# Kernel tuning notes

Measured on AMD Instinct MI355X. Metric: run time of the kernel, lower is better.

Reference implementation:

```python
import jax, jax.numpy as jnp
import numpy as np

B, CH, IMG, P = 16, 3, 384, 16
D, HEADS, DH, MLP, DEPTH = 384, 6, 64, 1536, 6
INNER = HEADS * DH
PD = P * P * 5 * CH          # SPT patch dim = 3840
GRID = IMG // P              # 24
NP = GRID * GRID             # 576 patches
SEQ = NP + 1                 # +cls = 577


def layer_norm(x, g, b, eps=1e-5):
    mu = jnp.mean(x, axis=-1, keepdims=True)
    var = jnp.var(x, axis=-1, keepdims=True)
    return (x - mu) * jax.lax.rsqrt(var + eps) * g + b


def spt_shifts(x):
    # F.pad semantics: (left,right,top,bottom) with negative = crop
    s1 = jnp.pad(x, ((0, 0), (0, 0), (0, 0), (1, 0)))[:, :, :, :-1]  # (1,-1,0,0)
    s2 = jnp.pad(x, ((0, 0), (0, 0), (0, 0), (0, 1)))[:, :, :, 1:]   # (-1,1,0,0)
    s3 = jnp.pad(x, ((0, 0), (0, 0), (1, 0), (0, 0)))[:, :, :-1, :]  # (0,0,1,-1)
    s4 = jnp.pad(x, ((0, 0), (0, 0), (0, 1), (0, 0)))[:, :, 1:, :]   # (0,0,-1,1)
    return jnp.concatenate([x, s1, s2, s3, s4], axis=1)  # [b, 5c, H, W]


def patchify(x):
    # 'b c (h p1) (w p2) -> b (h w) (p1 p2 c)'
    b, c, _, _ = x.shape
    x = x.reshape(b, c, GRID, P, GRID, P)
    x = x.transpose(0, 2, 4, 3, 5, 1)  # b h w p1 p2 c
    return x.reshape(b, GRID * GRID, P * P * c)


def setup_inputs():
    key = jax.random.key(0)
    ks = jax.random.split(key, 16)
    img = jax.random.normal(ks[0], (B, CH, IMG, IMG), jnp.float32)
    spt_g = jnp.ones((PD,), jnp.float32)
    spt_b = jnp.zeros((PD,), jnp.float32)
    spt_w = jax.random.normal(ks[1], (PD, D), jnp.float32) * (1.0 / np.sqrt(PD))
    spt_bias = jnp.zeros((D,), jnp.float32)
    pos = jax.random.normal(ks[2], (1, SEQ, D), jnp.float32) * 0.02
    cls = jax.random.normal(ks[3], (1, 1, D), jnp.float32) * 0.02
    attn_g = jnp.ones((DEPTH, D), jnp.float32)
    attn_b = jnp.zeros((DEPTH, D), jnp.float32)
    temp = jnp.full((DEPTH,), np.log(DH ** -0.5), jnp.float32)
    wqkv = jax.random.normal(ks[4], (DEPTH, D, 3 * INNER), jnp.float32) * 0.02
    wout = jax.random.normal(ks[5], (DEPTH, INNER, D), jnp.float32) * 0.02
    bout = jnp.zeros((DEPTH, D), jnp.float32)
    ff_g = jnp.ones((DEPTH, D), jnp.float32)
    ff_b = jnp.zeros((DEPTH, D), jnp.float32)
    w1 = jax.random.normal(ks[6], (DEPTH, D, MLP), jnp.float32) * 0.02
    b1 = jnp.zeros((DEPTH, MLP), jnp.float32)
    w2 = jax.random.normal(ks[7], (DEPTH, MLP, D), jnp.float32) * 0.02
    b2 = jnp.zeros((DEPTH, D), jnp.float32)
    return {"img": img, "spt_g": spt_g, "spt_b": spt_b, "spt_w": spt_w,
            "spt_bias": spt_bias, "pos": pos, "cls": cls, "attn_g": attn_g,
            "attn_b": attn_b, "temp": temp, "wqkv": wqkv, "wout": wout,
            "bout": bout, "ff_g": ff_g, "ff_b": ff_b, "w1": w1, "b1": b1,
            "w2": w2, "b2": b2}


def vit_forward(img, spt_g, spt_b, spt_w, spt_bias, pos, cls, attn_g, attn_b,
                temp, wqkv, wout, bout, ff_g, ff_b, w1, b1, w2, b2):
    # SPT patch embedding
    x = patchify(spt_shifts(img))                      # [b, NP, PD]
    x = layer_norm(x, spt_g, spt_b) @ spt_w + spt_bias  # [b, NP, D]
    b = x.shape[0]
    cls_tok = jnp.broadcast_to(cls, (b, 1, D))
    x = jnp.concatenate([cls_tok, x], axis=1) + pos[:, :SEQ]

    eye = jnp.eye(SEQ, dtype=bool)
    neg = -jnp.finfo(x.dtype).max

    def block(x, p):
        ag, ab, t, wq, wo, bo, fg, fb, W1, B1, W2, B2 = p
        h = layer_norm(x, ag, ab)
        qkv = h @ wq                                   # [b, n, 3*inner]
        q, k, v = jnp.split(qkv, 3, axis=-1)
        q = q.reshape(b, SEQ, HEADS, DH).transpose(0, 2, 1, 3)
        k = k.reshape(b, SEQ, HEADS, DH).transpose(0, 2, 1, 3)
        v = v.reshape(b, SEQ, HEADS, DH).transpose(0, 2, 1, 3)
        dots = jnp.einsum('bhid,bhjd->bhij', q, k) * jnp.exp(t)
        dots = jnp.where(eye, neg, dots)               # diagonal mask (LSA)
        attn = jax.nn.softmax(dots, axis=-1)
        out = jnp.einsum('bhij,bhjd->bhid', attn, v)
        out = out.transpose(0, 2, 1, 3).reshape(b, SEQ, INNER)
        x = out @ wo + bo + x
        h = layer_norm(x, fg, fb)
        x = jax.nn.gelu(h @ W1 + B1, approximate=False) @ W2 + B2 + x
        return x, None

    params = (attn_g, attn_b, temp, wqkv, wout, bout, ff_g, ff_b, w1, b1, w2, b2)
    x, _ = jax.lax.scan(block, x, params)
    return x


def reference(img, spt_g, spt_b, spt_w, spt_bias, pos, cls, attn_g, attn_b,
              temp, wqkv, wout, bout, ff_g, ff_b, w1, b1, w2, b2):
    return vit_forward(img, spt_g, spt_b, spt_w, spt_bias, pos, cls, attn_g,
                       attn_b, temp, wqkv, wout, bout, ff_g, ff_b, w1, b1,
                       w2, b2)
```

## Files before the change

### kernel.cpp

```cpp
#include <hip/hip_runtime.h>

typedef unsigned short ushort_t;
typedef __bf16 bf16x8 __attribute__((ext_vector_type(8)));
typedef float f32x4 __attribute__((ext_vector_type(4)));

#define SEQ_ 577
#define D_ 384
#define NTOK (16 * 577)

enum { M_QKV = 0, M_OUT, M_MLP1, M_MLP2 };

__device__ inline float b2f(ushort_t u) {
    unsigned int x = ((unsigned int)u) << 16;
    float f; __builtin_memcpy(&f, &x, 4); return f;
}
__device__ inline ushort_t f2b(float f) {
    unsigned int x; __builtin_memcpy(&x, &f, 4);
    x = x + 0x7fffu + ((x >> 16) & 1u);
    return (ushort_t)(x >> 16);
}

__device__ void transpose_tile(const float* __restrict__ src,
                               ushort_t* __restrict__ dst,
                               int ldn, int ldk, int k0, int n0)
{
    __shared__ float t[64][65];
    const int tid = threadIdx.x;
    const int c = tid & 63, rr = tid >> 6;
#pragma unroll
    for (int i = 0; i < 16; i++) {
        int kl = rr + i * 4;
        t[kl][c] = src[(size_t)(k0 + kl) * ldn + n0 + c];
    }
    __syncthreads();
#pragma unroll
    for (int i = 0; i < 16; i++) {
        int nl = rr + i * 4;
        dst[(size_t)(n0 + nl) * ldk + k0 + c] = f2b(t[c][nl]);
    }
}

__global__ __launch_bounds__(256) void prep_spt_kernel(
    const float* __restrict__ w, ushort_t* __restrict__ wt)
{
    transpose_tile(w, wt, 384, 3840, blockIdx.x * 64, blockIdx.y * 64);
}

__global__ __launch_bounds__(256) void prep_all_kernel(
    const float* __restrict__ wqkv, const float* __restrict__ wout,
    const float* __restrict__ w1, const float* __restrict__ w2,
    ushort_t* __restrict__ W6)
{
    int id = blockIdx.x;
    int l = id / 432;
    int r = id - l * 432;
    ushort_t* qkv_t  = W6 + (size_t)l * 1769472;
    ushort_t* wout_t = qkv_t + 442368;
    ushort_t* w1_t   = wout_t + 147456;
    ushort_t* w2_t   = w1_t + 589824;
    const float* wq = wqkv + (size_t)l * 442368;
    const float* wo = wout + (size_t)l * 147456;
    const float* W1 = w1 + (size_t)l * 589824;
    const float* W2 = w2 + (size_t)l * 589824;
    if (r < 108) {
        int kt = r / 18, nt = r % 18;
        transpose_tile(wq, qkv_t, 1152, 384, kt * 64, nt * 64);
    } else if (r < 144) {
        r -= 108; int kt = r / 6, nt = r % 6;
        transpose_tile(wo, wout_t, 384, 384, kt * 64, nt * 64);
    } else if (r < 288) {
        r -= 144; int kt = r / 24, nt = r % 24;
        transpose_tile(W1, w1_t, 1536, 384, kt * 64, nt * 64);
    } else {
        r -= 288; int kt = r / 6, nt = r % 6;
        transpose_tile(W2, w2_t, 384, 1536, kt * 64, nt * 64);
    }
}

template <int MODE>
__global__ __launch_bounds__(256) void gemm64(
    const ushort_t* __restrict__ A, const ushort_t* __restrict__ Bt,
    ushort_t* __restrict__ Co, float* __restrict__ resid,
    const float* __restrict__ bias,
    int M, int K, int ldc)
{
    __shared__ __align__(16) ushort_t As[2][64][40];
    __shared__ __align__(16) ushort_t Bs[2][64][40];

    const int tid = threadIdx.x;
    const int rowBase = blockIdx.y * 64;
    const int colBase = blockIdx.x * 64;
    const int nk = K >> 5;
    const int lr = tid >> 2, lk = (tid & 3) * 8;
    const int wv = tid >> 6, lane = tid & 63;
    const int wm = (wv >> 1) * 32, wn = (wv & 1) * 32;
    const int m16 = lane & 15, q4 = lane >> 4, kb = q4 * 8;

    const ushort_t* pa = A + (size_t)(rowBase + lr) * K + lk;
    const ushort_t* pb = Bt + (size_t)(colBase + lr) * K + lk;

    f32x4 acc[2][2];
#pragma unroll
    for (int i = 0; i < 2; i++)
#pragma unroll
        for (int j = 0; j < 2; j++) acc[i][j] = (f32x4){0.f, 0.f, 0.f, 0.f};

    uint4 Ua, Ub, Va, Vb;
    auto gloadU = [&](int kt) {
        Ua = *(const uint4*)(pa + kt * 32);
        Ub = *(const uint4*)(pb + kt * 32);
    };
    auto gloadV = [&](int kt) {
        Va = *(const uint4*)(pa + kt * 32);
        Vb = *(const uint4*)(pb + kt * 32);
    };
    auto swriteU = [&](int buf) {
        *(uint4*)&As[buf][lr][lk] = Ua;
        *(uint4*)&Bs[buf][lr][lk] = Ub;
    };
    auto swriteV = [&](int buf) {
        *(uint4*)&As[buf][lr][lk] = Va;
        *(uint4*)&Bs[buf][lr][lk] = Vb;
    };
    auto compute = [&](int buf) {
        bf16x8 a0 = *(const bf16x8*)&As[buf][wm + m16][kb];
        bf16x8 a1 = *(const bf16x8*)&As[buf][wm + 16 + m16][kb];
        bf16x8 b0 = *(const bf16x8*)&Bs[buf][wn + m16][kb];
        bf16x8 b1 = *(const bf16x8*)&Bs[buf][wn + 16 + m16][kb];
        acc[0][0] = __builtin_amdgcn_mfma_f32_16x16x32_bf16(a0, b0, acc[0][0], 0, 0, 0);
        acc[0][1] = __builtin_amdgcn_mfma_f32_16x16x32_bf16(a0, b1, acc[0][1], 0, 0, 0);
        acc[1][0] = __builtin_amdgcn_mfma_f32_16x16x32_bf16(a1, b0, acc[1][0], 0, 0, 0);
        acc[1][1] = __builtin_amdgcn_mfma_f32_16x16x32_bf16(a1, b1, acc[1][1], 0, 0, 0);
    };

    gloadU(0);
    swriteU(0);
    gloadU(1);
    gloadV(2);
    __syncthreads();

    for (int kt = 0; kt < nk; kt += 2) {
        swriteU(1);
        if (kt + 3 < nk) gloadU(kt + 3);
        compute(0);
        __syncthreads();
        if (kt + 2 < nk) {
            swriteV(0);
            if (kt + 4 < nk) gloadV(kt + 4);
        }
        compute(1);
        __syncthreads();
    }

#pragma unroll
    for (int im = 0; im < 2; im++)
#pragma unroll
        for (int in = 0; in < 2; in++) {
            int col = colBase + wn + in * 16 + m16;
#pragma unroll
            for (int r = 0; r < 4; r++) {
                int row = rowBase + wm + im * 16 + q4 * 4 + r;
                if (row >= M) continue;
                float v = acc[im][in][r];
                if (MODE == M_QKV) {
                    Co[(size_t)row * ldc + col] = f2b(v);
                } else if (MODE == M_MLP1) {
                    float t = v + bias[col];
                    float gl = 0.5f * t * (1.0f + erff(t * 0.70710678118f));
                    Co[(size_t)row * ldc + col] = f2b(gl);
                } else {
                    size_t o = (size_t)row * ldc + col;
                    resid[o] = resid[o] + v + bias[col];
                }
            }
        }
}

__global__ __launch_bounds__(256) void gemm64_spt(
    const ushort_t* __restrict__ A, const ushort_t* __restrict__ Bt,
    float* __restrict__ resid, const float* __restrict__ bias,
    const float* __restrict__ pos, int M, int K, int rowOff)
{
    __shared__ __align__(16) ushort_t As[64][40];
    __shared__ __align__(16) ushort_t Bs[64][40];

    const int tid = threadIdx.x;
    const int rowBase = blockIdx.y * 64;
    const int colBase = blockIdx.x * 64;
    const int nk = K >> 5;
    const int lr = tid >> 2, lk = (tid & 3) * 8;
    const int wv = tid >> 6, lane = tid & 63;
    const int wm = (wv >> 1) * 32, wn = (wv & 1) * 32;
    const int m16 = lane & 15, q4 = lane >> 4, kb = q4 * 8;

    const ushort_t* pa = A + (size_t)(rowBase + lr) * K + lk;
    const ushort_t* pb = Bt + (size_t)(colBase + lr) * K + lk;

    f32x4 acc[2][2];
#pragma unroll
    for (int i = 0; i < 2; i++)
#pragma unroll
        for (int j = 0; j < 2; j++) acc[i][j] = (f32x4){0.f, 0.f, 0.f, 0.f};

    uint4 xa = *(const uint4*)pa,        xb = *(const uint4*)pb;
    uint4 ya = *(const uint4*)(pa + 32), yb = *(const uint4*)(pb + 32);

    auto stage = [&](uint4& ra, uint4& rb, int ktNext) {
        __syncthreads();
        *(uint4*)&As[lr][lk] = ra;
        *(uint4*)&Bs[lr][lk] = rb;
        __syncthreads();
        if (ktNext < nk) {
            int off = ktNext * 32;
            ra = *(const uint4*)(pa + off);
            rb = *(const uint4*)(pb + off);
        }
        bf16x8 a0 = *(const bf16x8*)&As[wm + m16][kb];
        bf16x8 a1 = *(const bf16x8*)&As[wm + 16 + m16][kb];
        bf16x8 b0 = *(const bf16x8*)&Bs[wn + m16][kb];
        bf16x8 b1 = *(const bf16x8*)&Bs[wn + 16 + m16][kb];
        acc[0][0] = __builtin_amdgcn_mfma_f32_16x16x32_bf16(a0, b0, acc[0][0], 0, 0, 0);
        acc[0][1] = __builtin_amdgcn_mfma_f32_16x16x32_bf16(a0, b1, acc[0][1], 0, 0, 0);
        acc[1][0] = __builtin_amdgcn_mfma_f32_16x16x32_bf16(a1, b0, acc[1][0], 0, 0, 0);
        acc[1][1] = __builtin_amdgcn_mfma_f32_16x16x32_bf16(a1, b1, acc[1][1], 0, 0, 0);
    };

    for (int kt = 0; kt < nk; kt += 2) {
        stage(xa, xb, kt + 2);
        stage(ya, yb, kt + 3);
    }

#pragma unroll
    for (int im = 0; im < 2; im++)
#pragma unroll
        for (int in = 0; in < 2; in++) {
            int col = colBase + wn + in * 16 + m16;
#pragma unroll
            for (int r = 0; r < 4; r++) {
                int row = rowBase + wm + im * 16 + q4 * 4 + r;
                if (row >= M) continue;
                int grow = rowOff + row;
                int bb = grow / 576, p = grow - bb * 576;
                size_t o = ((size_t)(bb * SEQ_ + 1 + p)) * D_ + col;
                resid[o] = acc[im][in][r] + bias[col] + pos[(size_t)(1 + p) * D_ + col];
            }
        }
}

__global__ __launch_bounds__(256) void attn_kernel(
    const ushort_t* __restrict__ qkv, ushort_t* __restrict__ attn,
    const float* __restrict__ temp, int layer)
{
    const int qt = blockIdx.x;
    const int bh = blockIdx.y;
    const int b = bh / 6, hd = bh - b * 6;
    const int tid = threadIdx.x;
    const int wv = tid >> 6, lane = tid & 63;
    const int m16 = lane & 15, q4 = lane >> 4;
    const float sc2 = expf(temp[layer]) * 1.44269504f;

    __shared__ __align__(16) ushort_t Ks[64][72];
    __shared__ __align__(16) ushort_t Vt[64][72];
    __shared__ __align__(16) ushort_t Pw[4][16][72];

    const int qrow = qt * 64 + wv * 16 + m16;
    const int qtok = qrow < SEQ_ ? qrow : SEQ_ - 1;
    const ushort_t* qb = qkv + ((size_t)(b * SEQ_ + qtok)) * 1152 + hd * 64;
    bf16x8 qf0 = *(const bf16x8*)(qb + q4 * 8);
    bf16x8 qf1 = *(const bf16x8*)(qb + 32 + q4 * 8);

    f32x4 accO[4];
#pragma unroll
    for (int dt = 0; dt < 4; dt++) accO[dt] = (f32x4){0.f, 0.f, 0.f, 0.f};
    float l_r[4] = {0.f, 0.f, 0.f, 0.f};

    const int skey = tid >> 2;
    const int scol = (tid & 3) * 16;
    const int vp   = tid & 31;
    const int vdh  = (tid >> 5) * 8;

    for (int kt = 0; kt < 10; kt++) {
        int key = kt * 64 + skey;
        int gkey = key < SEQ_ ? key : 0;
        const ushort_t* kb_ = qkv + ((size_t)(b * SEQ_ + gkey)) * 1152 + 384 + hd * 64;
        uint4 kv0 = *(const uint4*)(kb_ + scol);
        uint4 kv1 = *(const uint4*)(kb_ + scol + 8);
        if (key >= SEQ_) { kv0 = (uint4){0, 0, 0, 0}; kv1 = kv0; }
        int vk0 = kt * 64 + 2 * vp;
        int t0 = vk0 < SEQ_ ? vk0 : 0;
        int t1 = vk0 + 1 < SEQ_ ? vk0 + 1 : 0;
        uint4 va = *(const uint4*)(qkv + ((size_t)(b * SEQ_ + t0)) * 1152 + 768 + hd * 64 + vdh);
        uint4 vb2 = *(const uint4*)(qkv + ((size_t)(b * SEQ_ + t1)) * 1152 + 768 + hd * 64 + vdh);
        if (vk0 >= SEQ_) va = (uint4){0, 0, 0, 0};
        if (vk0 + 1 >= SEQ_) vb2 = (uint4){0, 0, 0, 0};
        __syncthreads();
        *(uint4*)&Ks[skey][scol] = kv0;
        *(uint4*)&Ks[skey][scol + 8] = kv1;
        {
            const ushort_t* e0 = (const ushort_t*)&va;
            const ushort_t* e1 = (const ushort_t*)&vb2;
#pragma unroll
            for (int j = 0; j < 8; j++) {
                unsigned int pack = (unsigned int)e0[j] | ((unsigned int)e1[j] << 16);
                *(unsigned int*)&Vt[vdh + j][2 * vp] = pack;
            }
        }
        __syncthreads();

        f32x4 s[4];
#pragma unroll
        for (int ct = 0; ct < 4; ct++) {
            bf16x8 b0 = *(const bf16x8*)&Ks[ct * 16 + m16][q4 * 8];
            bf16x8 b1 = *(const bf16x8*)&Ks[ct * 16 + m16][32 + q4 * 8];
            f32x4 z = (f32x4){0.f, 0.f, 0.f, 0.f};
            z = __builtin_amdgcn_mfma_f32_16x16x32_bf16(qf0, b0, z, 0, 0, 0);
            z = __builtin_amdgcn_mfma_f32_16x16x32_bf16(qf1, b1, z, 0, 0, 0);
            s[ct] = z;
        }
        const int rowb = qt * 64 + wv * 16 + q4 * 4;
#pragma unroll
        for (int r = 0; r < 4; r++) {
            float rs = 0.f;
#pragma unroll
            for (int ct = 0; ct < 4; ct++) {
                int col = kt * 64 + ct * 16 + m16;
                float v = s[ct][r] * sc2;
                if (col >= SEQ_ || col == rowb + r) v = -1.0e30f;
                float p = __builtin_amdgcn_exp2f(v);
                s[ct][r] = p;
                rs += p;
            }
            rs += __shfl_xor(rs, 1);
            rs += __shfl_xor(rs, 2);
            rs += __shfl_xor(rs, 4);
            rs += __shfl_xor(rs, 8);
            l_r[r] += rs;
        }
#pragma unroll
        for (int ct = 0; ct < 4; ct++)
#pragma unroll
            for (int r = 0; r < 4; r++)
                Pw[wv][q4 * 4 + r][ct * 16 + m16] = f2b(s[ct][r]);
        bf16x8 pf0 = *(const bf16x8*)&Pw[wv][m16][q4 * 8];
        bf16x8 pf1 = *(const bf16x8*)&Pw[wv][m16][32 + q4 * 8];
#pragma unroll
        for (int dt = 0; dt < 4; dt++) {
            bf16x8 vb0 = *(const bf16x8*)&Vt[dt * 16 + m16][q4 * 8];
            bf16x8 vb1 = *(const bf16x8*)&Vt[dt * 16 + m16][32 + q4 * 8];
            f32x4 o = accO[dt];
            o = __builtin_amdgcn_mfma_f32_16x16x32_bf16(pf0, vb0, o, 0, 0, 0);
            o = __builtin_amdgcn_mfma_f32_16x16x32_bf16(pf1, vb1, o, 0, 0, 0);
            accO[dt] = o;
        }
    }

    const int rowb = qt * 64 + wv * 16 + q4 * 4;
#pragma unroll
    for (int r = 0; r < 4; r++) {
        int grow = rowb + r;
        if (grow >= SEQ_) continue;
        float inv = 1.f / l_r[r];
        ushort_t* op = attn + ((size_t)(b * SEQ_ + grow)) * 384 + hd * 64;
#pragma unroll
        for (int dt = 0; dt < 4; dt++)
            op[dt * 16 + m16] = f2b(accO[dt][r] * inv);
    }
}

__global__ __launch_bounds__(256) void spt_ln_kernel(
    const float* __restrict__ img, const float* __restrict__ gg,
    const float* __restrict__ bb_, ushort_t* __restrict__ Xn, int r0)
{
    int bp = r0 + blockIdx.x;
    int b = bp / 576, p = bp - b * 576;
    int ph = p / 24, pw = p - ph * 24;

    __shared__ float vals[3840];
    __shared__ float red[10];

    const int tid = threadIdx.x;
    const int p1 = tid >> 4, p2 = tid & 15;

    float s = 0.f, sq = 0.f;
#pragma unroll
    for (int plane = 0; plane < 15; plane++) {
        int g5 = plane / 3, ch = plane - g5 * 3;
        int row = ph * 16 + p1, col = pw * 16 + p2;
        if (g5 == 1) col -= 1;
        else if (g5 == 2) col += 1;
        else if (g5 == 3) row -= 1;
        else if (g5 == 4) row += 1;
        float v = 0.f;
        if (row >= 0 && row < 384 && col >= 0 && col < 384)
            v = img[((size_t)(b * 3 + ch) * 384 + row) * 384 + col];
        vals[tid * 15 + plane] = v;
        s += v; sq += v * v;
    }
#pragma unroll
    for (int off = 32; off > 0; off >>= 1) {
        s += __shfl_xor(s, off);
        sq += __shfl_xor(sq, off);
    }
    int wid = tid >> 6;
    if ((tid & 63) == 0) { red[wid] = s; red[4 + wid] = sq; }
    __syncthreads();
    if (tid == 0) {
        float S = red[0] + red[1] + red[2] + red[3];
        float Q = red[4] + red[5] + red[6] + red[7];
        float mean = S / 3840.f;
        float var = Q / 3840.f - mean * mean;
        red[8] = mean;
        red[9] = rsqrtf(var + 1e-5f);
    }
    __syncthreads();
    float mean = red[8], rstd = red[9];
#pragma unroll
    for (int i = 0; i < 15; i++) {
        int k = tid + i * 256;
        float v = (vals[k] - mean) * rstd * gg[k] + bb_[k];
        Xn[(size_t)blockIdx.x * 3840 + k] = f2b(v);
    }
}

__global__ __launch_bounds__(256) void ln_kernel(
    const float* __restrict__ x, const float* __restrict__ g,
    const float* __restrict__ b, ushort_t* __restrict__ h)
{
    int row = blockIdx.x * 4 + (threadIdx.x >> 6);
    int lane = threadIdx.x & 63;
    const float4* xr = (const float4*)(x + (size_t)row * 384);
    float4 a = xr[lane];
    float4 c = (lane < 32) ? xr[64 + lane] : make_float4(0.f, 0.f, 0.f, 0.f);
    float s = a.x + a.y + a.z + a.w + c.x + c.y + c.z + c.w;
    float sq = a.x * a.x + a.y * a.y + a.z * a.z + a.w * a.w
             + c.x * c.x + c.y * c.y + c.z * c.z + c.w * c.w;
#pragma unroll
    for (int off = 32; off > 0; off >>= 1) {
        s += __shfl_xor(s, off);
        sq += __shfl_xor(sq, off);
    }
    float mean = s / 384.f;
    float var = sq / 384.f - mean * mean;
    float rstd = rsqrtf(var + 1e-5f);
    const float4* g4 = (const float4*)g;
    const float4* b4 = (const float4*)b;
    ushort_t* hr = h + (size_t)row * 384;
    {
        float4 gv = g4[lane], bv = b4[lane];
        unsigned int lo = (unsigned int)f2b((a.x - mean) * rstd * gv.x + bv.x)
                        | ((unsigned int)f2b((a.y - mean) * rstd * gv.y + bv.y) << 16);
        unsigned int hi = (unsigned int)f2b((a.z - mean) * rstd * gv.z + bv.z)
                        | ((unsigned int)f2b((a.w - mean) * rstd * gv.w + bv.w) << 16);
        *(uint2*)&hr[lane * 4] = make_uint2(lo, hi);
    }
    if (lane < 32) {
        float4 gv = g4[64 + lane], bv = b4[64 + lane];
        unsigned int lo = (unsigned int)f2b((c.x - mean) * rstd * gv.x + bv.x)
                        | ((unsigned int)f2b((c.y - mean) * rstd * gv.y + bv.y) << 16);
        unsigned int hi = (unsigned int)f2b((c.z - mean) * rstd * gv.z + bv.z)
                        | ((unsigned int)f2b((c.w - mean) * rstd * gv.w + bv.w) << 16);
        *(uint2*)&hr[256 + lane * 4] = make_uint2(lo, hi);
    }
}

__global__ void cls_kernel(const float* __restrict__ cls,
                           const float* __restrict__ pos, float* __restrict__ x)
{
    int b = blockIdx.x, d = threadIdx.x;
    x[(size_t)b * SEQ_ * D_ + d] = cls[d] + pos[d];
}

extern "C" void kernel_launch(void* const* d_in, const int* in_sizes, int n_in,
                              void* d_out, int out_size, void* d_ws, size_t ws_size,
                              hipStream_t stream)
{
    const float* img      = (const float*)d_in[0];
    const float* spt_g    = (const float*)d_in[1];
    const float* spt_b    = (const float*)d_in[2];
    const float* spt_w    = (const float*)d_in[3];
    const float* spt_bias = (const float*)d_in[4];
    const float* pos      = (const float*)d_in[5];
    const float* clsp     = (const float*)d_in[6];
    const float* attn_g   = (const float*)d_in[7];
    const float* attn_b   = (const float*)d_in[8];
    const float* temp     = (const float*)d_in[9];
    const float* wqkv     = (const float*)d_in[10];
    const float* wout     = (const float*)d_in[11];
    const float* bout     = (const float*)d_in[12];
    const float* ff_g     = (const float*)d_in[13];
    const float* ff_b     = (const float*)d_in[14];
    const float* w1       = (const float*)d_in[15];
    const float* b1       = (const float*)d_in[16];
    const float* w2       = (const float*)d_in[17];
    const float* b2       = (const float*)d_in[18];

    float* x = (float*)d_out;

    char* base = (char*)d_ws;
    ushort_t* qkv   = (ushort_t*)base;
    ushort_t* attn  = (ushort_t*)(base + (size_t)NTOK * 1152 * 2);
    ushort_t* Xn    = (ushort_t*)base;
    ushort_t* gbuf  = (ushort_t*)base;
    ushort_t* spt_wt = (ushort_t*)(base + 23592960);
    char* p2 = base + (size_t)NTOK * 1536 * 2;
    ushort_t* h  = (ushort_t*)p2;
    char* p3 = p2 + (size_t)NTOK * 384 * 2;
    ushort_t* W6 = (ushort_t*)p3;

    prep_all_kernel<<<2592, 256, 0, stream>>>(wqkv, wout, w1, w2, W6);
    prep_spt_kernel<<<dim3(60, 6), 256, 0, stream>>>(spt_w, spt_wt);

    for (int c = 0; c < 3; c++) {
        int r0 = c * 3072;
        spt_ln_kernel<<<3072, 256, 0, stream>>>(img, spt_g, spt_b, Xn, r0);
        gemm64_spt<<<dim3(6, 48), 256, 0, stream>>>(
            Xn, spt_wt, x, spt_bias, pos, 3072, 3840, r0);
    }
    cls_kernel<<<16, 384, 0, stream>>>(clsp, pos, x);

    for (int l = 0; l < 6; l++) {
        ushort_t* qkv_t  = W6 + (size_t)l * 1769472;
        ushort_t* wout_t = qkv_t + 442368;
        ushort_t* w1_t   = wout_t + 147456;
        ushort_t* w2_t   = w1_t + 589824;
        ln_kernel<<<NTOK / 4, 256, 0, stream>>>(x, attn_g + l * 384, attn_b + l * 384, h);
        gemm64<M_QKV><<<dim3(18, 145), 256, 0, stream>>>(
            h, qkv_t, qkv, nullptr, nullptr, NTOK, 384, 1152);
        attn_kernel<<<dim3(10, 96), 256, 0, stream>>>(qkv, attn, temp, l);
        gemm64<M_OUT><<<dim3(6, 145), 256, 0, stream>>>(
            attn, wout_t, nullptr, x, bout + l * 384, NTOK, 384, 384);
        ln_kernel<<<NTOK / 4, 256, 0, stream>>>(x, ff_g + l * 384, ff_b + l * 384, h);
        gemm64<M_MLP1><<<dim3(24, 145), 256, 0, stream>>>(
            h, w1_t, gbuf, nullptr, b1 + l * 1536, NTOK, 384, 1536);
        gemm64<M_MLP2><<<dim3(6, 145), 256, 0, stream>>>(
            gbuf, w2_t, nullptr, x, b2 + l * 384, NTOK, 1536, 384);
    }
}
```

Before: 1.317 ms.

## Split-K the SPT GEMM with atomics, double-buffer it, and XCD-swizzle GEMM blocks

The SPT patch-embedding GEMM is split four ways along K (3840), growing its grid from 288 to 1152 blocks, and partial sums are combined with float atomicAdd into x. A new init kernel pre-fills x with bias+pos for patch rows and cls+pos for the cls row. The split kernel also moves to a double-buffered LDS pipeline with a single barrier per stage. All GEMMs remap block IDs so consecutive blocks scheduled on the same XCD cover neighbouring tiles for better L2 reuse. The atomics make the summation order nondeterministic and add atomic traffic, and the split kernel hardcodes K and the grid shape.

Measured after the change: 1.202 ms. 1.1x faster.

```diff
diff --git a/kernel.cpp b/kernel.cpp
--- a/kernel.cpp
+++ b/kernel.cpp
@@ -87,9 +87,17 @@
     __shared__ __align__(16) ushort_t As[2][64][40];
     __shared__ __align__(16) ushort_t Bs[2][64][40];
 
+    const int gx = gridDim.x;
+    const int nwg = gx * gridDim.y;
+    const int f = blockIdx.y * gx + blockIdx.x;
+    const int q = nwg >> 3, rr_ = nwg & 7;
+    const int xcd = f & 7, ii = f >> 3;
+    const int swz = (xcd < rr_ ? xcd * (q + 1) : rr_ * (q + 1) + (xcd - rr_) * q) + ii;
+    const int bx = swz % gx, by = swz / gx;
+
     const int tid = threadIdx.x;
-    const int rowBase = blockIdx.y * 64;
-    const int colBase = blockIdx.x * 64;
+    const int rowBase = by * 64;
+    const int colBase = bx * 64;
     const int nk = K >> 5;
     const int lr = tid >> 2, lk = (tid & 3) * 8;
     const int wv = tid >> 6, lane = tid & 63;
@@ -176,25 +184,32 @@
         }
 }
 
-__global__ __launch_bounds__(256) void gemm64_spt(
+__global__ __launch_bounds__(256) void gemm64_spt_split(
     const ushort_t* __restrict__ A, const ushort_t* __restrict__ Bt,
-    float* __restrict__ resid, const float* __restrict__ bias,
-    const float* __restrict__ pos, int M, int K, int rowOff)
-{
-    __shared__ __align__(16) ushort_t As[64][40];
-    __shared__ __align__(16) ushort_t Bs[64][40];
+    float* __restrict__ resid, int rowOff)
+{
+    __shared__ __align__(16) ushort_t As[2][64][40];
+    __shared__ __align__(16) ushort_t Bs[2][64][40];
+
+    const int f = blockIdx.z * 288 + blockIdx.y * 6 + blockIdx.x;
+    const int swz = (f & 7) * 144 + (f >> 3);
+    const int bz = swz / 288;
+    const int rem = swz - bz * 288;
+    const int by = rem / 6, bx = rem - by * 6;
+
+    const int K = 3840, nk = 30;
+    const int rowBase = by * 64;
+    const int colBase = bx * 64;
+    const int kbase = bz * 960;
 
     const int tid = threadIdx.x;
-    const int rowBase = blockIdx.y * 64;
-    const int colBase = blockIdx.x * 64;
-    const int nk = K >> 5;
     const int lr = tid >> 2, lk = (tid & 3) * 8;
     const int wv = tid >> 6, lane = tid & 63;
     const int wm = (wv >> 1) * 32, wn = (wv & 1) * 32;
     const int m16 = lane & 15, q4 = lane >> 4, kb = q4 * 8;
 
-    const ushort_t* pa = A + (size_t)(rowBase + lr) * K + lk;
-    const ushort_t* pb = Bt + (size_t)(colBase + lr) * K + lk;
+    const ushort_t* pa = A + (size_t)(rowBase + lr) * K + kbase + lk;
+    const ushort_t* pb = Bt + (size_t)(colBase + lr) * K + kbase + lk;
 
     f32x4 acc[2][2];
 #pragma unroll
@@ -202,32 +217,51 @@
 #pragma unroll
         for (int j = 0; j < 2; j++) acc[i][j] = (f32x4){0.f, 0.f, 0.f, 0.f};
 
-    uint4 xa = *(const uint4*)pa,        xb = *(const uint4*)pb;
-    uint4 ya = *(const uint4*)(pa + 32), yb = *(const uint4*)(pb + 32);
-
-    auto stage = [&](uint4& ra, uint4& rb, int ktNext) {
-        __syncthreads();
-        *(uint4*)&As[lr][lk] = ra;
-        *(uint4*)&Bs[lr][lk] = rb;
-        __syncthreads();
-        if (ktNext < nk) {
-            int off = ktNext * 32;
-            ra = *(const uint4*)(pa + off);
-            rb = *(const uint4*)(pb + off);
-        }
-        bf16x8 a0 = *(const bf16x8*)&As[wm + m16][kb];
-        bf16x8 a1 = *(const bf16x8*)&As[wm + 16 + m16][kb];
-        bf16x8 b0 = *(const bf16x8*)&Bs[wn + m16][kb];
-        bf16x8 b1 = *(const bf16x8*)&Bs[wn + 16 + m16][kb];
+    uint4 Ua, Ub, Va, Vb;
+    auto gloadU = [&](int kt) {
+        Ua = *(const uint4*)(pa + kt * 32);
+        Ub = *(const uint4*)(pb + kt * 32);
+    };
+    auto gloadV = [&](int kt) {
+        Va = *(const uint4*)(pa + kt * 32);
+        Vb = *(const uint4*)(pb + kt * 32);
+    };
+    auto swriteU = [&](int buf) {
+        *(uint4*)&As[buf][lr][lk] = Ua;
+        *(uint4*)&Bs[buf][lr][lk] = Ub;
+    };
+    auto swriteV = [&](int buf) {
+        *(uint4*)&As[buf][lr][lk] = Va;
+        *(uint4*)&Bs[buf][lr][lk] = Vb;
+    };
+    auto compute = [&](int buf) {
+        bf16x8 a0 = *(const bf16x8*)&As[buf][wm + m16][kb];
+        bf16x8 a1 = *(const bf16x8*)&As[buf][wm + 16 + m16][kb];
+        bf16x8 b0 = *(const bf16x8*)&Bs[buf][wn + m16][kb];
+        bf16x8 b1 = *(const bf16x8*)&Bs[buf][wn + 16 + m16][kb];
         acc[0][0] = __builtin_amdgcn_mfma_f32_16x16x32_bf16(a0, b0, acc[0][0], 0, 0, 0);
         acc[0][1] = __builtin_amdgcn_mfma_f32_16x16x32_bf16(a0, b1, acc[0][1], 0, 0, 0);
         acc[1][0] = __builtin_amdgcn_mfma_f32_16x16x32_bf16(a1, b0, acc[1][0], 0, 0, 0);
         acc[1][1] = __builtin_amdgcn_mfma_f32_16x16x32_bf16(a1, b1, acc[1][1], 0, 0, 0);
     };
 
+    gloadU(0);
+    swriteU(0);
+    gloadU(1);
+    gloadV(2);
+    __syncthreads();
+
     for (int kt = 0; kt < nk; kt += 2) {
-        stage(xa, xb, kt + 2);
-        stage(ya, yb, kt + 3);
+        swriteU(1);
+        if (kt + 3 < nk) gloadU(kt + 3);
+        compute(0);
+        __syncthreads();
+        if (kt + 2 < nk) {
+            swriteV(0);
+            if (kt + 4 < nk) gloadV(kt + 4);
+        }
+        compute(1);
+        __syncthreads();
     }
 
 #pragma unroll
@@ -238,11 +272,10 @@
 #pragma unroll
             for (int r = 0; r < 4; r++) {
                 int row = rowBase + wm + im * 16 + q4 * 4 + r;
-                if (row >= M) continue;
                 int grow = rowOff + row;
                 int bb = grow / 576, p = grow - bb * 576;
                 size_t o = ((size_t)(bb * SEQ_ + 1 + p)) * D_ + col;
-                resid[o] = acc[im][in][r] + bias[col] + pos[(size_t)(1 + p) * D_ + col];
+                atomicAdd(&resid[o], acc[im][in][r]);
             }
         }
 }
@@ -463,11 +496,14 @@
     }
 }
 
-__global__ void cls_kernel(const float* __restrict__ cls,
-                           const float* __restrict__ pos, float* __restrict__ x)
-{
-    int b = blockIdx.x, d = threadIdx.x;
-    x[(size_t)b * SEQ_ * D_ + d] = cls[d] + pos[d];
+__global__ void init_x_kernel(const float* __restrict__ cls,
+                              const float* __restrict__ pos,
+                              const float* __restrict__ spt_bias,
+                              float* __restrict__ x)
+{
+    int s = blockIdx.x, b = blockIdx.y, d = threadIdx.x;
+    float base = (s == 0) ? cls[d] : spt_bias[d];
+    x[((size_t)b * SEQ_ + s) * D_ + d] = base + pos[(size_t)s * D_ + d];
 }
 
 extern "C" void kernel_launch(void* const* d_in, const int* in_sizes, int n_in,
@@ -509,14 +545,13 @@
 
     prep_all_kernel<<<2592, 256, 0, stream>>>(wqkv, wout, w1, w2, W6);
     prep_spt_kernel<<<dim3(60, 6), 256, 0, stream>>>(spt_w, spt_wt);
+    init_x_kernel<<<dim3(SEQ_, 16), 384, 0, stream>>>(clsp, pos, spt_bias, x);
 
     for (int c = 0; c < 3; c++) {
         int r0 = c * 3072;
         spt_ln_kernel<<<3072, 256, 0, stream>>>(img, spt_g, spt_b, Xn, r0);
-        gemm64_spt<<<dim3(6, 48), 256, 0, stream>>>(
-            Xn, spt_wt, x, spt_bias, pos, 3072, 3840, r0);
-    }
-    cls_kernel<<<16, 384, 0, stream>>>(clsp, pos, x);
+        gemm64_spt_split<<<dim3(6, 48, 4), 256, 0, stream>>>(Xn, spt_wt, x, r0);
+    }
 
     for (int l = 0; l < 6; l++) {
         ushort_t* qkv_t  = W6 + (size_t)l * 1769472;
```
